# Kernel tuning notes

Measured on AMD Instinct MI355X. Metric: run time of the kernel, lower is better.

The kernel has to match this reference:

```python
import jax, jax.numpy as jnp
import numpy as np

N_NODES = 20000
N_EDGES = 100000
WIDTH = 64
KER_IN = 6
KER_HID = WIDTH // 4  # 16
DEPTH = 6


def setup_inputs() -> dict:
    key = jax.random.key(0)
    ks = jax.random.split(key, 12)
    s = lambda fan_in: 1.0 / np.sqrt(fan_in)
    return {
        "x": jax.random.normal(ks[0], (N_NODES, 1), dtype=jnp.float32),
        "edge_index": jax.random.randint(ks[1], (2, N_EDGES), 0, N_NODES, dtype=jnp.int32),
        "edge_attr": jax.random.uniform(ks[2], (N_EDGES, KER_IN), dtype=jnp.float32),
        "fc1_w": jax.random.normal(ks[3], (1, WIDTH), dtype=jnp.float32) * s(1),
        "fc1_b": jnp.zeros((WIDTH,), dtype=jnp.float32),
        "k1_w": jax.random.normal(ks[4], (KER_IN, KER_HID), dtype=jnp.float32) * s(KER_IN),
        "k1_b": jnp.zeros((KER_HID,), dtype=jnp.float32),
        "k2_w": jax.random.normal(ks[5], (KER_HID, WIDTH * WIDTH), dtype=jnp.float32) * s(KER_HID),
        "k2_b": jnp.zeros((WIDTH * WIDTH,), dtype=jnp.float32),
        "root_w": jax.random.normal(ks[6], (WIDTH, WIDTH), dtype=jnp.float32) * s(WIDTH),
        "conv_b": jnp.zeros((WIDTH,), dtype=jnp.float32),
        "fc2_w": jax.random.normal(ks[7], (WIDTH, 1), dtype=jnp.float32) * s(WIDTH),
        "fc2_b": jnp.zeros((1,), dtype=jnp.float32),
    }


def reference(x, edge_index, edge_attr, fc1_w, fc1_b, k1_w, k1_b, k2_w, k2_b,
              root_w, conv_b, fc2_w, fc2_b):
    src = edge_index[0]  # source nodes j
    dst = edge_index[1]  # target nodes i

    # fc1: lift node features [N,1] -> [N,W]
    h = x @ fc1_w + fc1_b

    # Edge-conditioned weight matrices via kernel MLP (edge_attr is layer-invariant,
    # so compute once and reuse for all DEPTH layers — identical math).
    ek = jax.nn.relu(edge_attr @ k1_w + k1_b)           # [E, W/4]
    W = (ek @ k2_w + k2_b).reshape(N_EDGES, WIDTH, WIDTH)  # [E, W, W]

    # mean aggregation denominator (in-degree, clamped to avoid div-by-zero)
    deg = jax.ops.segment_sum(jnp.ones((N_EDGES,), dtype=h.dtype), dst,
                              num_segments=N_NODES)
    denom = jnp.maximum(deg, 1.0)[:, None]               # [N,1]

    for _ in range(DEPTH):
        # per-edge matmul: msg_e = x_src[e] @ W_e
        msg = jnp.einsum('ei,eio->eo', h[src], W)        # [E, W]
        agg = jax.ops.segment_sum(msg, dst, num_segments=N_NODES) / denom
        h = jax.nn.relu(agg + h @ root_w + conv_b)       # NNConv root weight + bias, then outer ReLU

    return h @ fc2_w + fc2_b                              # [N, 1]
```

## Files before the change

kernel.cpp:

```cpp
#include <hip/hip_runtime.h>
#include <hip/hip_bf16.h>


#define NN 20000
#define NE 100000
#define WD 64
#define DEPTH 6

typedef __attribute__((ext_vector_type(8))) short bf16x8;
typedef __attribute__((ext_vector_type(4))) float f32x4;

typedef __attribute__((address_space(1))) const void gvoid;
typedef __attribute__((address_space(3))) void lvoid;
__device__ __forceinline__ void gl_lds16(const void* g, void* l) {
    __builtin_amdgcn_global_load_lds((gvoid*)g, (lvoid*)l, 16, 0, 0);
}

__device__ __forceinline__ unsigned short f2bf(float v) {
    union { float f; unsigned u; } x; x.f = v;
    unsigned r = x.u + 0x7fffu + ((x.u >> 16) & 1u);
    return (unsigned short)(r >> 16);
}
__device__ __forceinline__ float bf2f(unsigned short b) {
    union { unsigned u; float f; } x; x.u = ((unsigned)b) << 16;
    return x.f;
}

__global__ __launch_bounds__(256) void count_kernel(const int* __restrict__ ei,
                                                    int* __restrict__ outc,
                                                    int* __restrict__ inc)
{
    int e = blockIdx.x * 256 + threadIdx.x;
    if (e >= NE) return;
    atomicAdd(&outc[ei[e]], 1);
    atomicAdd(&inc[ei[NE + e]], 1);
}

__global__ __launch_bounds__(256) void scanA_kernel(const int* __restrict__ cnt,
                                                    int* __restrict__ partials)
{
    int b = blockIdx.x, t = threadIdx.x, lane = t & 63, w = t >> 6;
    int base = b * 1024 + t * 4;
    int s = 0;
#pragma unroll
    for (int i = 0; i < 4; ++i) {
        int idx = base + i;
        if (idx < 2 * NN) s += cnt[idx];
    }
#pragma unroll
    for (int off = 32; off > 0; off >>= 1) s += __shfl_down(s, off, 64);
    __shared__ int wsum[4];
    if (lane == 0) wsum[w] = s;
    __syncthreads();
    if (t == 0) partials[b] = wsum[0] + wsum[1] + wsum[2] + wsum[3];
}

__global__ __launch_bounds__(64) void scanB_kernel(const int* __restrict__ partials,
                                                   int* __restrict__ bases)
{
    int l = threadIdx.x;
    int p = (l < 40) ? partials[l] : 0;
    int v = p;
#pragma unroll
    for (int off = 1; off < 64; off <<= 1) {
        int u = __shfl_up(v, off, 64);
        if (l >= off) v += u;
    }
    if (l < 40) bases[l] = v - p;
}

__global__ __launch_bounds__(256) void scanC_kernel(const int* __restrict__ cnt,
                                                    const int* __restrict__ bases,
                                                    int* __restrict__ rps,
                                                    int* __restrict__ rpd,
                                                    float* __restrict__ invd)
{
    int b = blockIdx.x, t = threadIdx.x, lane = t & 63, w = t >> 6;
    int base = b * 1024 + t * 4;
    int v[4], s = 0;
#pragma unroll
    for (int i = 0; i < 4; ++i) {
        int idx = base + i;
        v[i] = (idx < 2 * NN) ? cnt[idx] : 0;
        s += v[i];
    }
    int tsum = s, sc = s;
#pragma unroll
    for (int off = 1; off < 64; off <<= 1) {
        int u = __shfl_up(sc, off, 64);
        if (lane >= off) sc += u;
    }
    __shared__ int wtot[4];
    if (lane == 63) wtot[w] = sc;
    __syncthreads();
    int wbase = 0;
    for (int j = 0; j < w; ++j) wbase += wtot[j];
    int run = bases[b] + wbase + sc - tsum;
#pragma unroll
    for (int i = 0; i < 4; ++i) {
        int idx = base + i;
        int e = run; run += v[i];
        if (idx < NN) {
            rps[idx] = e;
        } else if (idx < 2 * NN) {
            rpd[idx - NN] = e - NE;
            invd[idx - NN] = 1.0f / fmaxf((float)v[i], 1.0f);
        }
    }
    if (b == 0 && t == 0) { rps[NN] = NE; rpd[NN] = NE; }
}

__global__ __launch_bounds__(256) void ekfill_kernel(
    const int* __restrict__ ei, const float* __restrict__ ea,
    const float* __restrict__ k1w, const float* __restrict__ k1b,
    const int* __restrict__ rpd, int* __restrict__ fd,
    float* __restrict__ eks, int* __restrict__ smeta)
{
    int e = blockIdx.x * 256 + threadIdx.x;
    if (e >= NE) return;
    int s = ei[e], d = ei[NE + e];
    float a[6];
#pragma unroll
    for (int i = 0; i < 6; ++i) a[i] = ea[e * 6 + i];
    int slot_d = rpd[d] + atomicAdd(&fd[d], 1);
    smeta[slot_d] = s;
#pragma unroll
    for (int j = 0; j < 16; ++j) {
        float v = k1b[j];
#pragma unroll
        for (int i = 0; i < 6; ++i) v = fmaf(a[i], k1w[i * 16 + j], v);
        eks[(size_t)slot_d * 16 + j] = fmaxf(v, 0.f);
    }
}

__global__ __launch_bounds__(256) void gwt2_kernel(
    const float* __restrict__ k2w, const float* __restrict__ k2b,
    const float* __restrict__ rootw,
    unsigned short* __restrict__ K2qh, unsigned short* __restrict__ K2ql,
    unsigned short* __restrict__ Rqh, unsigned short* __restrict__ Rql)
{
    int idx = blockIdx.x * 256 + threadIdx.x;
    if (idx >= 64 * 1152) return;
    int o = idx / 1152, j = idx - o * 1152;
    float g;
    if (j < 1024)      { int c = j >> 6, k = j & 63; g = k2w[c * 4096 + k * 64 + o]; }
    else if (j < 1088) { int k = j - 1024;           g = k2b[k * 64 + o]; }
    else               { int k = j - 1088;           g = rootw[k * 64 + o]; }
    unsigned short hi = f2bf(g);
    unsigned short lo = f2bf(g - bf2f(hi));
    if (j < 1088) { K2qh[o * 1088 + j] = hi; K2ql[o * 1088 + j] = lo; }
    else { int k = j - 1088; Rqh[o * 64 + k] = hi; Rql[o * 64 + k] = lo; }
}

__global__ __launch_bounds__(256) void h0_kernel(
    const float* __restrict__ x, const float* __restrict__ w,
    const float* __restrict__ b, float* __restrict__ h,
    unsigned short* __restrict__ hhi, unsigned short* __restrict__ hlo)
{
    int idx = blockIdx.x * 256 + threadIdx.x;
    if (idx >= NN * WD) return;
    int n = idx >> 6, o = idx & 63;
    float v = fmaf(x[n], w[o], b[o]);
    h[idx] = v;
    unsigned short hi = f2bf(v);
    hhi[idx] = hi;
    hlo[idx] = f2bf(v - bf2f(hi));
}

__global__ __launch_bounds__(256) void ucomp_kernel(
    const float* __restrict__ h, const float* __restrict__ eks,
    const int* __restrict__ smeta, const int* __restrict__ rpd,
    unsigned short* __restrict__ Uhi, unsigned short* __restrict__ Ulo,
    int nbase, int nend)
{
    int wv = threadIdx.x >> 6;
    int i = nbase + blockIdx.x * 4 + wv;
    if (i >= nend) return;
    int l = threadIdx.x & 63;
    float acc[17];
#pragma unroll
    for (int c = 0; c < 17; ++c) acc[c] = 0.f;
    int r0 = rpd[i], r1 = rpd[i + 1];
    if (r0 < r1) {
        int su = __builtin_amdgcn_readfirstlane(r0);
        float hv = h[(size_t)smeta[su] * 64 + l];
        const float* er = eks + (size_t)su * 16;
        f32x4 e0 = *(const f32x4*)(er);
        f32x4 e1 = *(const f32x4*)(er + 4);
        f32x4 e2 = *(const f32x4*)(er + 8);
        f32x4 e3 = *(const f32x4*)(er + 12);
        for (int s = r0; s < r1; ++s) {
            float ch = hv;
            f32x4 c0 = e0, c1 = e1, c2 = e2, c3 = e3;
            if (s + 1 < r1) {
                int s2 = __builtin_amdgcn_readfirstlane(s + 1);
                hv = h[(size_t)smeta[s2] * 64 + l];
                const float* er2 = eks + (size_t)s2 * 16;
                e0 = *(const f32x4*)(er2);
                e1 = *(const f32x4*)(er2 + 4);
                e2 = *(const f32x4*)(er2 + 8);
                e3 = *(const f32x4*)(er2 + 12);
            }
            acc[0]  = fmaf(c0[0], ch, acc[0]);
            acc[1]  = fmaf(c0[1], ch, acc[1]);
            acc[2]  = fmaf(c0[2], ch, acc[2]);
            acc[3]  = fmaf(c0[3], ch, acc[3]);
            acc[4]  = fmaf(c1[0], ch, acc[4]);
            acc[5]  = fmaf(c1[1], ch, acc[5]);
            acc[6]  = fmaf(c1[2], ch, acc[6]);
            acc[7]  = fmaf(c1[3], ch, acc[7]);
            acc[8]  = fmaf(c2[0], ch, acc[8]);
            acc[9]  = fmaf(c2[1], ch, acc[9]);
            acc[10] = fmaf(c2[2], ch, acc[10]);
            acc[11] = fmaf(c2[3], ch, acc[11]);
            acc[12] = fmaf(c3[0], ch, acc[12]);
            acc[13] = fmaf(c3[1], ch, acc[13]);
            acc[14] = fmaf(c3[2], ch, acc[14]);
            acc[15] = fmaf(c3[3], ch, acc[15]);
            acc[16] += ch;
        }
    }
    size_t ub = (size_t)(i - nbase) * 1088 + l;
#pragma unroll
    for (int c = 0; c < 17; ++c) {
        unsigned short hi = f2bf(acc[c]);
        Uhi[ub + c * 64] = hi;
        Ulo[ub + c * 64] = f2bf(acc[c] - bf2f(hi));
    }
}

__global__ __launch_bounds__(512, 6) void ugemm_kernel(
    const unsigned short* __restrict__ Uhi, const unsigned short* __restrict__ Ulo,
    const unsigned short* __restrict__ K2qh, const unsigned short* __restrict__ K2ql,
    const unsigned short* __restrict__ Rqh, const unsigned short* __restrict__ Rql,
    const unsigned short* __restrict__ hhi_in, const unsigned short* __restrict__ hlo_in,
    const float* __restrict__ invd, const float* __restrict__ convb,
    float* __restrict__ h_out, unsigned short* __restrict__ hhi_out,
    unsigned short* __restrict__ hlo_out, int nbase, int nend)
{
    __shared__ __align__(16) unsigned short Asm[2][8][2][32][8];
    __shared__ __align__(16) unsigned short Bsm[2][8][2][64][8];
    int tid = threadIdx.x;
    int w = tid >> 6, l = tid & 63;
    int quad = l >> 4, lr = l & 15;
    int rg = w >> 2, ct = w & 3;
    int n0 = nbase + blockIdx.x * 32;
    int n0l = n0 - nbase;
    int ncl = nend - nbase;

    int ga = tid >> 6, ha = (tid >> 5) & 1, ra = tid & 31;
    int rla = n0l + ra; if (rla >= ncl) rla = ncl - 1;
    const unsigned short* asrc = (ha ? Ulo : Uhi) + (size_t)rla * 1088 + ga * 8;
    int gb0 = tid >> 7, hb0 = (tid >> 6) & 1, ob0 = tid & 63;
    int ub1 = 512 + tid;
    int gb1 = ub1 >> 7, hb1 = (ub1 >> 6) & 1, ob1 = ub1 & 63;
    const unsigned short* bsrc0 = (hb0 ? K2ql : K2qh) + (size_t)ob0 * 1088 + gb0 * 8;
    const unsigned short* bsrc1 = (hb1 ? K2ql : K2qh) + (size_t)ob1 * 1088 + gb1 * 8;

    gl_lds16(asrc, (void*)&Asm[0][ga][ha][ra][0]);
    gl_lds16(bsrc0, (void*)&Bsm[0][gb0][hb0][ob0][0]);
    gl_lds16(bsrc1, (void*)&Bsm[0][gb1][hb1][ob1][0]);
    __syncthreads();

    int r = rg * 16 + lr;
    int o = ct * 16 + lr;
    f32x4 acc = {0.f, 0.f, 0.f, 0.f};
    int cur = 0;
    for (int c = 0; c < 17; ++c) {
        if (c + 1 < 17) {
            int koff = (c + 1) * 64;
            int nb = cur ^ 1;
            gl_lds16(asrc + koff, (void*)&Asm[nb][ga][ha][ra][0]);
            gl_lds16(bsrc0 + koff, (void*)&Bsm[nb][gb0][hb0][ob0][0]);
            gl_lds16(bsrc1 + koff, (void*)&Bsm[nb][gb1][hb1][ob1][0]);
        }
#pragma unroll
        for (int kk = 0; kk < 2; ++kk) {
            int g = kk * 4 + quad;
            bf16x8 ah = *(const bf16x8*)&Asm[cur][g][0][r][0];
            bf16x8 av = *(const bf16x8*)&Asm[cur][g][1][r][0];
            bf16x8 bh = *(const bf16x8*)&Bsm[cur][g][0][o][0];
            bf16x8 bl = *(const bf16x8*)&Bsm[cur][g][1][o][0];
            acc = __builtin_amdgcn_mfma_f32_16x16x32_bf16(ah, bh, acc, 0, 0, 0);
            acc = __builtin_amdgcn_mfma_f32_16x16x32_bf16(ah, bl, acc, 0, 0, 0);
            acc = __builtin_amdgcn_mfma_f32_16x16x32_bf16(av, bh, acc, 0, 0, 0);
        }
        __syncthreads();
        cur ^= 1;
    }

    int row = n0 + rg * 16 + lr;
    if (row > nend - 1) row = nend - 1;
    f32x4 r0a = {0.f, 0.f, 0.f, 0.f};
    const unsigned short* prh = hhi_in + (size_t)row * 64 + quad * 8;
    const unsigned short* prl = hlo_in + (size_t)row * 64 + quad * 8;
#pragma unroll
    for (int ks = 0; ks < 2; ++ks) {
        bf16x8 ah = *(const bf16x8*)(prh + ks * 32);
        bf16x8 av = *(const bf16x8*)(prl + ks * 32);
        bf16x8 bh = *(const bf16x8*)(Rqh + (size_t)o * 64 + ks * 32 + quad * 8);
        bf16x8 bl = *(const bf16x8*)(Rql + (size_t)o * 64 + ks * 32 + quad * 8);
        r0a = __builtin_amdgcn_mfma_f32_16x16x32_bf16(ah, bh, r0a, 0, 0, 0);
        r0a = __builtin_amdgcn_mfma_f32_16x16x32_bf16(ah, bl, r0a, 0, 0, 0);
        r0a = __builtin_amdgcn_mfma_f32_16x16x32_bf16(av, bh, r0a, 0, 0, 0);
    }
    float cb0 = convb[o];
#pragma unroll
    for (int rr = 0; rr < 4; ++rr) {
        int gn = n0 + rg * 16 + quad * 4 + rr;
        if (gn < nend) {
            float iv = invd[gn];
            size_t idx0 = (size_t)gn * 64 + o;
            float v0 = fmaf(acc[rr], iv, r0a[rr] + cb0);
            v0 = fmaxf(v0, 0.f);
            h_out[idx0] = v0;
            unsigned short x0 = f2bf(v0);
            hhi_out[idx0] = x0;
            hlo_out[idx0] = f2bf(v0 - bf2f(x0));
        }
    }
}

__global__ __launch_bounds__(256) void out_kernel(
    const float* __restrict__ h, const float* __restrict__ fc2_w,
    const float* __restrict__ fc2_b, float* __restrict__ out)
{
    int wave = blockIdx.x * 4 + (threadIdx.x >> 6);
    int lane = threadIdx.x & 63;
    float v = h[(size_t)wave * 64 + lane] * fc2_w[lane];
#pragma unroll
    for (int off = 32; off > 0; off >>= 1) v += __shfl_down(v, off);
    if (lane == 0) out[wave] = v + fc2_b[0];
}

extern "C" void kernel_launch(void* const* d_in, const int* in_sizes, int n_in,
                              void* d_out, int out_size, void* d_ws, size_t ws_size,
                              hipStream_t stream)
{
    const float* x         = (const float*)d_in[0];
    const int*   ei        = (const int*)  d_in[1];
    const float* edge_attr = (const float*)d_in[2];
    const float* fc1_w     = (const float*)d_in[3];
    const float* fc1_b     = (const float*)d_in[4];
    const float* k1_w      = (const float*)d_in[5];
    const float* k1_b      = (const float*)d_in[6];
    const float* k2_w      = (const float*)d_in[7];
    const float* k2_b      = (const float*)d_in[8];
    const float* root_w    = (const float*)d_in[9];
    const float* conv_b    = (const float*)d_in[10];
    const float* fc2_w     = (const float*)d_in[11];
    const float* fc2_b     = (const float*)d_in[12];
    float* out = (float*)d_out;

    float* ws = (float*)d_ws;
    size_t off = 0;
    int* cnt   = (int*)(ws + off); off += 4 * NN;
    int* outc  = cnt;
    int* inc   = cnt + NN;
    int* fd    = cnt + 3 * NN;
    int* rps   = (int*)(ws + off); off += 20004;
    int* rpd   = (int*)(ws + off); off += 20004;
    int* partials = (int*)(ws + off); off += 64;
    int* bases    = (int*)(ws + off); off += 64;
    int* smeta    = (int*)(ws + off); off += NE + 16;
    float* invd  = ws + off; off += NN;
    float* eks   = ws + off; off += (size_t)NE * 16;
    unsigned short* K2qh = (unsigned short*)(ws + off); off += 34816;
    unsigned short* K2ql = (unsigned short*)(ws + off); off += 34816;
    unsigned short* Rqh  = (unsigned short*)(ws + off); off += 2048;
    unsigned short* Rql  = (unsigned short*)(ws + off); off += 2048;
    float* hA    = ws + off; off += (size_t)NN * WD;
    float* hB    = ws + off; off += (size_t)NN * WD;
    unsigned short* hhiA = (unsigned short*)(ws + off); off += (size_t)NN * 32;
    unsigned short* hloA = (unsigned short*)(ws + off); off += (size_t)NN * 32;
    unsigned short* hhiB = (unsigned short*)(ws + off); off += (size_t)NN * 32;
    unsigned short* hloB = (unsigned short*)(ws + off); off += (size_t)NN * 32;

    size_t totalf = ws_size / sizeof(float);
    size_t availf = totalf > off ? totalf - off : 0;
    const int divs[] = {1, 2, 4, 5, 8, 10, 20};
    int nch = 20;
    for (int di = 0; di < 7; ++di) {
        if (availf >= (size_t)(NN / divs[di]) * 1088) { nch = divs[di]; break; }
    }
    int csz = NN / nch;
    unsigned short* Uhi = (unsigned short*)(ws + off);
    unsigned short* Ulo = (unsigned short*)(ws + off + (size_t)csz * 544);

    hipMemsetAsync(cnt, 0, 4 * NN * sizeof(int), stream);
    count_kernel<<<(NE + 255) / 256, 256, 0, stream>>>(ei, outc, inc);
    scanA_kernel<<<40, 256, 0, stream>>>(cnt, partials);
    scanB_kernel<<<1, 64, 0, stream>>>(partials, bases);
    scanC_kernel<<<40, 256, 0, stream>>>(cnt, bases, rps, rpd, invd);
    ekfill_kernel<<<(NE + 255) / 256, 256, 0, stream>>>(ei, edge_attr, k1_w, k1_b,
                                                        rpd, fd, eks, smeta);
    gwt2_kernel<<<(64 * 1152 + 255) / 256, 256, 0, stream>>>(k2_w, k2_b, root_w,
                                                             K2qh, K2ql, Rqh, Rql);
    h0_kernel<<<(NN * WD + 255) / 256, 256, 0, stream>>>(x, fc1_w, fc1_b,
                                                         hA, hhiA, hloA);

    const float* hin = hA; float* hout = hB;
    const unsigned short* hhin = hhiA; const unsigned short* hloin = hloA;
    unsigned short* hhout = hhiB; unsigned short* hloout = hloB;
    for (int layer = 0; layer < DEPTH; ++layer) {
        for (int c = 0; c < nch; ++c) {
            int nb = c * csz, ne2 = nb + csz;
            ucomp_kernel<<<(csz + 3) / 4, 256, 0, stream>>>(
                hin, eks, smeta, rpd, Uhi, Ulo, nb, ne2);
            ugemm_kernel<<<(csz + 31) / 32, 512, 0, stream>>>(
                Uhi, Ulo, K2qh, K2ql, Rqh, Rql, hhin, hloin, invd, conv_b,
                hout, hhout, hloout, nb, ne2);
        }
        const float* t0 = hin; hin = hout; hout = (float*)t0;
        const unsigned short* t1 = hhin; hhin = hhout; hhout = (unsigned short*)t1;
        const unsigned short* t2 = hloin; hloin = hloout; hloout = (unsigned short*)t2;
    }

    out_kernel<<<NN / 4, 256, 0, stream>>>(hin, fc2_w, fc2_b, out);
}
```

Measured before the change: 565.7 us.

## Shrink ugemm tile to 16 rows and read K2 weights directly from global

The ugemm kernel now processes 16 nodes per 256-thread block instead of 32 nodes per 512-thread block. It drops the LDS staging of the K2 weight tiles, so each wave loads its B fragments straight from global memory, where they should hit in cache. Only the U tile stays double-buffered in LDS. This lowers LDS use and cuts load instructions per block, but each block now re-reads K2 from L2 with less reuse. Separately, ucomp swaps readfirstlane for an inline v_mov into a VGPR for the edge index, which may change how the scalar and vector loads are scheduled.

```diff
diff --git a/kernel.cpp b/kernel.cpp
--- a/kernel.cpp
+++ b/kernel.cpp
@@ -14,6 +14,9 @@
 typedef __attribute__((address_space(3))) void lvoid;
 __device__ __forceinline__ void gl_lds16(const void* g, void* l) {
     __builtin_amdgcn_global_load_lds((gvoid*)g, (lvoid*)l, 16, 0, 0);
+}
+__device__ __forceinline__ int to_vgpr(int s) {
+    int v; asm("v_mov_b32 %0, %1" : "=v"(v) : "s"(s)); return v;
 }
 
 __device__ __forceinline__ unsigned short f2bf(float v) {
@@ -182,7 +185,7 @@
     for (int c = 0; c < 17; ++c) acc[c] = 0.f;
     int r0 = rpd[i], r1 = rpd[i + 1];
     if (r0 < r1) {
-        int su = __builtin_amdgcn_readfirstlane(r0);
+        int su = to_vgpr(r0);
         float hv = h[(size_t)smeta[su] * 64 + l];
         const float* er = eks + (size_t)su * 16;
         f32x4 e0 = *(const f32x4*)(er);
@@ -193,7 +196,7 @@
             float ch = hv;
             f32x4 c0 = e0, c1 = e1, c2 = e2, c3 = e3;
             if (s + 1 < r1) {
-                int s2 = __builtin_amdgcn_readfirstlane(s + 1);
+                int s2 = to_vgpr(s + 1);
                 hv = h[(size_t)smeta[s2] * 64 + l];
                 const float* er2 = eks + (size_t)s2 * 16;
                 e0 = *(const f32x4*)(er2);
@@ -229,7 +232,7 @@
     }
 }
 
-__global__ __launch_bounds__(512, 6) void ugemm_kernel(
+__global__ __launch_bounds__(256, 6) void ugemm_kernel(
     const unsigned short* __restrict__ Uhi, const unsigned short* __restrict__ Ulo,
     const unsigned short* __restrict__ K2qh, const unsigned short* __restrict__ K2ql,
     const unsigned short* __restrict__ Rqh, const unsigned short* __restrict__ Rql,
@@ -238,49 +241,38 @@
     float* __restrict__ h_out, unsigned short* __restrict__ hhi_out,
     unsigned short* __restrict__ hlo_out, int nbase, int nend)
 {
-    __shared__ __align__(16) unsigned short Asm[2][8][2][32][8];
-    __shared__ __align__(16) unsigned short Bsm[2][8][2][64][8];
+    __shared__ __align__(16) unsigned short Asm[2][8][2][16][8];
     int tid = threadIdx.x;
     int w = tid >> 6, l = tid & 63;
     int quad = l >> 4, lr = l & 15;
-    int rg = w >> 2, ct = w & 3;
-    int n0 = nbase + blockIdx.x * 32;
+    int n0 = nbase + blockIdx.x * 16;
     int n0l = n0 - nbase;
     int ncl = nend - nbase;
 
-    int ga = tid >> 6, ha = (tid >> 5) & 1, ra = tid & 31;
+    int ga = tid >> 5, ha = (tid >> 4) & 1, ra = tid & 15;
     int rla = n0l + ra; if (rla >= ncl) rla = ncl - 1;
     const unsigned short* asrc = (ha ? Ulo : Uhi) + (size_t)rla * 1088 + ga * 8;
-    int gb0 = tid >> 7, hb0 = (tid >> 6) & 1, ob0 = tid & 63;
-    int ub1 = 512 + tid;
-    int gb1 = ub1 >> 7, hb1 = (ub1 >> 6) & 1, ob1 = ub1 & 63;
-    const unsigned short* bsrc0 = (hb0 ? K2ql : K2qh) + (size_t)ob0 * 1088 + gb0 * 8;
-    const unsigned short* bsrc1 = (hb1 ? K2ql : K2qh) + (size_t)ob1 * 1088 + gb1 * 8;
 
     gl_lds16(asrc, (void*)&Asm[0][ga][ha][ra][0]);
-    gl_lds16(bsrc0, (void*)&Bsm[0][gb0][hb0][ob0][0]);
-    gl_lds16(bsrc1, (void*)&Bsm[0][gb1][hb1][ob1][0]);
     __syncthreads();
 
-    int r = rg * 16 + lr;
-    int o = ct * 16 + lr;
+    int o = w * 16 + lr;
+    const unsigned short* pbh = K2qh + (size_t)o * 1088 + quad * 8;
+    const unsigned short* pbl = K2ql + (size_t)o * 1088 + quad * 8;
     f32x4 acc = {0.f, 0.f, 0.f, 0.f};
     int cur = 0;
     for (int c = 0; c < 17; ++c) {
-        if (c + 1 < 17) {
-            int koff = (c + 1) * 64;
-            int nb = cur ^ 1;
-            gl_lds16(asrc + koff, (void*)&Asm[nb][ga][ha][ra][0]);
-            gl_lds16(bsrc0 + koff, (void*)&Bsm[nb][gb0][hb0][ob0][0]);
-            gl_lds16(bsrc1 + koff, (void*)&Bsm[nb][gb1][hb1][ob1][0]);
-        }
+        if (c + 1 < 17)
+            gl_lds16(asrc + (size_t)(c + 1) * 64,
+                     (void*)&Asm[cur ^ 1][ga][ha][ra][0]);
+        int kb = c * 64;
 #pragma unroll
         for (int kk = 0; kk < 2; ++kk) {
             int g = kk * 4 + quad;
-            bf16x8 ah = *(const bf16x8*)&Asm[cur][g][0][r][0];
-            bf16x8 av = *(const bf16x8*)&Asm[cur][g][1][r][0];
-            bf16x8 bh = *(const bf16x8*)&Bsm[cur][g][0][o][0];
-            bf16x8 bl = *(const bf16x8*)&Bsm[cur][g][1][o][0];
+            bf16x8 ah = *(const bf16x8*)&Asm[cur][g][0][lr][0];
+            bf16x8 av = *(const bf16x8*)&Asm[cur][g][1][lr][0];
+            bf16x8 bh = *(const bf16x8*)(pbh + kb + kk * 32);
+            bf16x8 bl = *(const bf16x8*)(pbl + kb + kk * 32);
             acc = __builtin_amdgcn_mfma_f32_16x16x32_bf16(ah, bh, acc, 0, 0, 0);
             acc = __builtin_amdgcn_mfma_f32_16x16x32_bf16(ah, bl, acc, 0, 0, 0);
             acc = __builtin_amdgcn_mfma_f32_16x16x32_bf16(av, bh, acc, 0, 0, 0);
@@ -289,7 +281,7 @@
         cur ^= 1;
     }
 
-    int row = n0 + rg * 16 + lr;
+    int row = n0 + lr;
     if (row > nend - 1) row = nend - 1;
     f32x4 r0a = {0.f, 0.f, 0.f, 0.f};
     const unsigned short* prh = hhi_in + (size_t)row * 64 + quad * 8;
@@ -307,7 +299,7 @@
     float cb0 = convb[o];
 #pragma unroll
     for (int rr = 0; rr < 4; ++rr) {
-        int gn = n0 + rg * 16 + quad * 4 + rr;
+        int gn = n0 + quad * 4 + rr;
         if (gn < nend) {
             float iv = invd[gn];
             size_t idx0 = (size_t)gn * 64 + o;
@@ -407,7 +399,7 @@
             int nb = c * csz, ne2 = nb + csz;
             ucomp_kernel<<<(csz + 3) / 4, 256, 0, stream>>>(
                 hin, eks, smeta, rpd, Uhi, Ulo, nb, ne2);
-            ugemm_kernel<<<(csz + 31) / 32, 512, 0, stream>>>(
+            ugemm_kernel<<<(csz + 15) / 16, 256, 0, stream>>>(
                 Uhi, Ulo, K2qh, K2ql, Rqh, Rql, hhin, hloin, invd, conv_b,
                 hout, hhout, hloout, nb, ne2);
         }
```

After: 633.8 us. 12.0% more time.
